# Optimization experiments

Measured on AMD Instinct MI355X. Metric: run time of the kernel, lower is better.

Reference implementation:

```python
import jax, jax.numpy as jnp
import numpy as np

SLOPE = 0.2  # leaky_relu_slope for both LVC block and kernel predictor (passed through)
DILATIONS = (1, 3, 9, 27)
HOP = 256
STRIDE = 8
IN_CH = 32
KSZ = 3  # conv_kernel_size


def conv1d(x, w, b, dilation=1, padding=0):
    # x: (B,C,T), w: (O,I,K) torch layout
    y = jax.lax.conv_general_dilated(
        x, w, window_strides=(1,), padding=[(padding, padding)],
        rhs_dilation=(dilation,), dimension_numbers=('NCH', 'OIH', 'NCH'))
    return y + b[None, :, None]


def conv_transpose1d(x, w, b, stride, padding, output_padding=0):
    # w: torch ConvTranspose1d layout (Cin, Cout, K)
    w_ = jnp.flip(w, -1).transpose(1, 0, 2)  # (Cout, Cin, K)
    K = w.shape[2]
    pad = (K - 1 - padding, K - 1 - padding + output_padding)
    y = jax.lax.conv_general_dilated(
        x, w_, window_strides=(1,), padding=[pad],
        lhs_dilation=(stride,), dimension_numbers=('NCH', 'OIH', 'NCH'))
    return y + b[None, :, None]


def lrelu(x, slope=SLOPE):
    return jnp.where(x >= 0, x, slope * x)


def location_variable_convolution(x, kernel, bias, hop):
    # x: (B,C,T), kernel: (B,C,O,k,L), bias: (B,O,L); T == L*hop; dilation==1 path
    B, C, T = x.shape
    _, _, O, k, L = kernel.shape
    pad = (k - 1) // 2
    xp = jnp.pad(x, ((0, 0), (0, 0), (pad, pad)))
    # gather per-segment sliding windows: (L, hop, k) index into time axis
    idx = (jnp.arange(L)[:, None, None] * hop
           + jnp.arange(hop)[None, :, None]
           + jnp.arange(k)[None, None, :])
    xw = xp[:, :, idx]  # (B, C, L, hop, k)
    o = jnp.einsum('bclsk,bcokl->bols', xw, kernel)  # (B, O, L, hop)
    o = o + bias[:, :, :, None]
    return o.reshape(B, O, L * hop)


def kernel_predictor(spec, kp_in_w, kp_in_b, rb_w1, rb_b1, rb_w2, rb_b2,
                     kern_w, kern_b, bias_w, bias_b):
    B, _, L = spec.shape
    h = conv1d(spec, kp_in_w, kp_in_b, padding=2)  # k=5, pad=2
    for i in range(3):  # num_blocks = 3
        r = h
        h = conv1d(h, rb_w1[i], rb_b1[i], padding=1)
        h = lrelu(h)
        h = conv1d(h, rb_w2[i], rb_b2[i], padding=1)
        h = lrelu(h) + r
    kh = conv1d(h, kern_w, kern_b, padding=1)
    bh = conv1d(h, bias_w, bias_b, padding=1)
    n_layers = len(DILATIONS)
    kernels = kh.reshape(B, n_layers, IN_CH, 2 * IN_CH, KSZ, L)
    biases = bh.reshape(B, n_layers, 2 * IN_CH, L)
    return kernels, biases


def reference(hidden_states, spectrogram, convt_w, convt_b, kp_in_w, kp_in_b,
              rb_w1, rb_b1, rb_w2, rb_b2, kern_w, kern_b, bias_w, bias_b,
              lvc_w, lvc_b):
    h = conv_transpose1d(hidden_states, convt_w, convt_b,
                         stride=STRIDE, padding=STRIDE // 2 + STRIDE % 2,
                         output_padding=STRIDE % 2)
    kernels, biases = kernel_predictor(spectrogram, kp_in_w, kp_in_b,
                                       rb_w1, rb_b1, rb_w2, rb_b2,
                                       kern_w, kern_b, bias_w, bias_b)
    for i, d in enumerate(DILATIONS):
        r = h
        h = lrelu(h)
        h = conv1d(h, lvc_w[i], lvc_b[i], dilation=d, padding=d * (KSZ - 1) // 2)
        h = lrelu(h)
        h = location_variable_convolution(h, kernels[:, i], biases[:, i], HOP)
        h = jax.nn.sigmoid(h[:, :IN_CH, :]) * jnp.tanh(h[:, IN_CH:, :]) + r
    return h


def setup_inputs() -> dict:
    key = jax.random.key(0)
    ks = jax.random.split(key, 12)
    B, COND, L, H = 4, 100, 256, 64
    T = L * HOP  # 65536 output samples
    s = jnp.float32(0.02)
    d = {}
    d['hidden_states'] = jax.random.normal(ks[0], (B, IN_CH, T // STRIDE), jnp.float32)
    d['spectrogram'] = jax.random.normal(ks[1], (B, COND, L), jnp.float32)
    d['convt_w'] = jax.random.normal(ks[2], (IN_CH, IN_CH, 2 * STRIDE), jnp.float32) * s
    d['convt_b'] = jnp.zeros((IN_CH,), jnp.float32)
    d['kp_in_w'] = jax.random.normal(ks[3], (H, COND, 5), jnp.float32) * s
    d['kp_in_b'] = jnp.zeros((H,), jnp.float32)
    d['rb_w1'] = jax.random.normal(ks[4], (3, H, H, 3), jnp.float32) * s
    d['rb_b1'] = jnp.zeros((3, H), jnp.float32)
    d['rb_w2'] = jax.random.normal(ks[5], (3, H, H, 3), jnp.float32) * s
    d['rb_b2'] = jnp.zeros((3, H), jnp.float32)
    KC = IN_CH * 2 * IN_CH * KSZ * len(DILATIONS)  # 24576
    d['kern_w'] = jax.random.normal(ks[6], (KC, H, 3), jnp.float32) * s
    d['kern_b'] = jnp.zeros((KC,), jnp.float32)
    BC = 2 * IN_CH * len(DILATIONS)  # 256
    d['bias_w'] = jax.random.normal(ks[7], (BC, H, 3), jnp.float32) * s
    d['bias_b'] = jnp.zeros((BC,), jnp.float32)
    d['lvc_w'] = jax.random.normal(ks[8], (len(DILATIONS), IN_CH, IN_CH, 3), jnp.float32) * s
    d['lvc_b'] = jnp.zeros((len(DILATIONS), IN_CH), jnp.float32)
    return d
```

## Files before the change

kernel.cpp:

```cpp
#include <hip/hip_runtime.h>
#include <math.h>

#define NB 4
#define T 65536
#define TIN 8192
#define LL 256
#define KCL 6144

__device__ __forceinline__ float lrelu_f(float v) { return v >= 0.f ? v : 0.2f * v; }

union Phase1LDS {
    struct { float xs[32][264]; float wm[64][128]; } cvt;
    struct { float hs[64][56]; float xsp[20][56]; float wt[192][68]; } trk;
};

__global__ void __launch_bounds__(512) phase1(
    const float* __restrict__ x, const float* __restrict__ cw,
    const float* __restrict__ cbias, float* __restrict__ hout,
    const float* __restrict__ spec,
    const float* __restrict__ kp_in_w, const float* __restrict__ kp_in_b,
    const float* __restrict__ rb_w1, const float* __restrict__ rb_b1,
    const float* __restrict__ rb_w2, const float* __restrict__ rb_b2,
    float* __restrict__ kp_h) {
    __shared__ Phase1LDS u;
    const int bid = blockIdx.x;
    const int tid = threadIdx.x;
    const int lane = tid & 63, wv = tid >> 6;

    if (bid < 264) {
        const int bx = bid % 33;
        const int rr = bid / 33;
        const int mtp = rr & 1;
        const int b = rr >> 1;
        const int s0base = bx * 256;
        float (*xs)[264] = u.cvt.xs;
        float (*wm)[128] = u.cvt.wm;

        const float* xb = x + (size_t)b * 32 * TIN;
        for (int idx = tid; idx < 32 * 64; idx += 512) {
            int c = idx >> 6, q = idx & 63;
            int p = s0base + q * 4;
            float4 v = (p + 3 < TIN) ? *(const float4*)(xb + c * TIN + p)
                                     : make_float4(0.f, 0.f, 0.f, 0.f);
            *(float4*)&xs[c][4 + 4 * q] = v;
        }
        if (tid < 32) {
            int p = s0base - 1;
            xs[tid][3] = (p >= 0) ? xb[tid * TIN + p] : 0.f;
        }
        for (int idx = tid; idx < 8192; idx += 512) {
            int i = idx >> 7, mm = idx & 127;
            int oo = mtp * 16 + (mm >> 3), k0 = mm & 7;
            wm[i][mm] = (i < 32) ? cw[i * 512 + oo * 16 + k0]
                                 : cw[(i - 32) * 512 + oo * 16 + k0 + 8];
        }
        __syncthreads();

        float acc[2][8][4];
#pragma unroll
        for (int ol = 0; ol < 2; ++ol) {
            float bo = cbias[mtp * 16 + wv * 2 + ol];
#pragma unroll
            for (int k0 = 0; k0 < 8; ++k0)
#pragma unroll
                for (int si = 0; si < 4; ++si) acc[ol][k0][si] = bo;
        }

        for (int c = 0; c < 32; ++c) {
            float xm1[4], x0[4];
#pragma unroll
            for (int si = 0; si < 4; ++si) {
                xm1[si] = xs[c][lane + si * 64 + 3];
                x0[si]  = xs[c][lane + si * 64 + 4];
            }
            float w0[16], w1[16];
#pragma unroll
            for (int q = 0; q < 4; ++q) {
                *(float4*)&w0[q * 4] = *(const float4*)&wm[c][wv * 16 + q * 4];
                *(float4*)&w1[q * 4] = *(const float4*)&wm[32 + c][wv * 16 + q * 4];
            }
#pragma unroll
            for (int ol = 0; ol < 2; ++ol)
#pragma unroll
                for (int k0 = 0; k0 < 8; ++k0)
#pragma unroll
                    for (int si = 0; si < 4; ++si)
                        acc[ol][k0][si] += x0[si] * w0[ol * 8 + k0] + xm1[si] * w1[ol * 8 + k0];
        }

#pragma unroll
        for (int ol = 0; ol < 2; ++ol) {
            float* ob = hout + ((size_t)b * 32 + mtp * 16 + wv * 2 + ol) * T;
#pragma unroll
            for (int si = 0; si < 4; ++si) {
                int tb = (s0base + lane + si * 64) * 8 - 4;
                if (tb >= 0 && tb < T)
                    *(float4*)(ob + tb) = make_float4(acc[ol][0][si], acc[ol][1][si],
                                                      acc[ol][2][si], acc[ol][3][si]);
                if (tb + 4 >= 0 && tb + 4 < T)
                    *(float4*)(ob + tb + 4) = make_float4(acc[ol][4][si], acc[ol][5][si],
                                                          acc[ol][6][si], acc[ol][7][si]);
            }
        }
        return;
    }

    const int tb = bid - 264;
    const int lq = tb & 7, b = tb >> 3;
    const int j = lane;
    const int oc0 = wv * 8;
    const int l0 = lq * 32;
    const int labs = l0 - 9 + j;
    const bool lvalid = (labs >= 0 && labs < 256);

    float (*hs)[56] = u.trk.hs;
    float (*xsp)[56] = u.trk.xsp;
    float (*wt)[68] = u.trk.wt;

    float pw[24];
    float px[3];

    auto pf_kpin = [&](int cc) {
#pragma unroll
        for (int t = 0; t < 13; ++t) {
            int idx = t * 512 + tid;
            pw[t] = 0.f;
            if (idx < 6400) pw[t] = kp_in_w[(size_t)(idx / 100) * 500 + cc * 100 + (idx % 100)];
        }
    };
    auto wr_kpin = [&]() {
#pragma unroll
        for (int t = 0; t < 13; ++t) {
            int idx = t * 512 + tid;
            if (idx < 6400) wt[idx % 100][idx / 100] = pw[t];
        }
    };
    auto pf_xsp = [&](int cc) {
#pragma unroll
        for (int t = 0; t < 3; ++t) {
            int idx = t * 512 + tid;
            px[t] = 0.f;
            if (idx < 1120) {
                int c = idx / 56, jj = idx - c * 56;
                int l = l0 - 9 + jj;
                if (l >= 0 && l < 256)
                    px[t] = spec[((size_t)b * 100 + cc * 20 + c) * LL + l];
            }
        }
    };
    auto wr_xsp = [&]() {
#pragma unroll
        for (int t = 0; t < 3; ++t) {
            int idx = t * 512 + tid;
            if (idx < 1120) xsp[idx / 56][idx % 56] = px[t];
        }
    };
    auto pf_w192 = [&](const float* src) {
#pragma unroll
        for (int t = 0; t < 24; ++t) pw[t] = src[t * 512 + tid];
    };
    auto wr_w192 = [&]() {
#pragma unroll
        for (int t = 0; t < 24; ++t) {
            int idx = t * 512 + tid;
            wt[idx % 192][idx / 192] = pw[t];
        }
    };
    auto conv64 = [&](int jlo, int jhi, const float* bptr, float* a) {
#pragma unroll
        for (int oi = 0; oi < 8; ++oi) a[oi] = bptr[oc0 + oi];
        if (j >= jlo && j < jhi) {
            for (int c = 0; c < 64; ++c) {
                float x0 = hs[c][j - 1], x1 = hs[c][j], x2 = hs[c][j + 1];
#pragma unroll
                for (int k = 0; k < 3; ++k) {
                    float xk = (k == 0) ? x0 : (k == 1) ? x1 : x2;
                    float w8[8];
                    *(float4*)&w8[0] = *(const float4*)&wt[c * 3 + k][oc0];
                    *(float4*)&w8[4] = *(const float4*)&wt[c * 3 + k][oc0 + 4];
#pragma unroll
                    for (int oi = 0; oi < 8; ++oi) a[oi] += xk * w8[oi];
                }
            }
        }
    };

    pf_kpin(0); pf_xsp(0);
    wr_kpin(); wr_xsp();
    __syncthreads();

    float acc[8];
#pragma unroll
    for (int oi = 0; oi < 8; ++oi) acc[oi] = kp_in_b[oc0 + oi];

    for (int cc = 0; cc < 5; ++cc) {
        if (cc < 4) { pf_kpin(cc + 1); pf_xsp(cc + 1); }
        else        { pf_w192(rb_w1); }
        if (j >= 2 && j < 48) {
            for (int c = 0; c < 20; ++c) {
                float x5[5];
#pragma unroll
                for (int u2 = 0; u2 < 5; ++u2) x5[u2] = xsp[c][j - 2 + u2];
#pragma unroll
                for (int k = 0; k < 5; ++k) {
                    float w8[8];
                    *(float4*)&w8[0] = *(const float4*)&wt[c * 5 + k][oc0];
                    *(float4*)&w8[4] = *(const float4*)&wt[c * 5 + k][oc0 + 4];
#pragma unroll
                    for (int oi = 0; oi < 8; ++oi) acc[oi] += x5[k] * w8[oi];
                }
            }
        }
        if (cc == 4 && j >= 2 && j < 48) {
#pragma unroll
            for (int oi = 0; oi < 8; ++oi) hs[oc0 + oi][j] = lvalid ? acc[oi] : 0.f;
        }
        __syncthreads();
        if (cc < 4) { wr_kpin(); wr_xsp(); }
        else        { wr_w192(); }
        __syncthreads();
    }

    for (int i = 0; i < 3; ++i) {
        const int jlo1 = 3 + 2 * i, jhi1 = 47 - 2 * i;
        const int jlo2 = jlo1 + 1, jhi2 = jhi1 - 1;
        float r[8];
        if (j >= jlo2 && j < jhi2) {
#pragma unroll
            for (int oi = 0; oi < 8; ++oi) r[oi] = hs[oc0 + oi][j];
        }
        pf_w192(rb_w2 + (size_t)i * 12288);
        float a1[8];
        conv64(jlo1, jhi1, rb_b1 + i * 64, a1);
        __syncthreads();
        if (j >= jlo1 && j < jhi1) {
#pragma unroll
            for (int oi = 0; oi < 8; ++oi) hs[oc0 + oi][j] = lvalid ? lrelu_f(a1[oi]) : 0.f;
        }
        wr_w192();
        __syncthreads();
        if (i < 2) pf_w192(rb_w1 + (size_t)(i + 1) * 12288);
        float a2[8];
        conv64(jlo2, jhi2, rb_b2 + i * 64, a2);
        __syncthreads();
        if (j >= jlo2 && j < jhi2) {
#pragma unroll
            for (int oi = 0; oi < 8; ++oi) hs[oc0 + oi][j] = lvalid ? (lrelu_f(a2[oi]) + r[oi]) : 0.f;
        }
        if (i < 2) wr_w192();
        __syncthreads();
    }

    for (int idx = tid; idx < 64 * 32; idx += 512) {
        int c = idx >> 5, jj = idx & 31;
        kp_h[((size_t)b * 64 + c) * LL + l0 + jj] = hs[c][9 + jj];
    }
}

__global__ void __launch_bounds__(256, 3) kern_head(const float* __restrict__ kp_h,
                                                    const float* __restrict__ kw,
                                                    const float* __restrict__ kb,
                                                    const float* __restrict__ bias_w,
                                                    const float* __restrict__ bias_b,
                                                    float* __restrict__ kh,
                                                    float* __restrict__ bh, int layer) {
    const int bx = blockIdx.x, b = blockIdx.y;
    const bool isbias = (bx >= 192);
    const int tid = threadIdx.x, lane = tid & 63, wv = tid >> 6;
    __shared__ float xs[32][264];
    __shared__ float ws[96][36];

    int g = 0, oc0 = 0, ci = 0, kk = 0, ocb0 = 0;
    const float* wsrc;
    size_t wrow0;
    int wstride;
    if (!isbias) {
        g = bx >> 1; oc0 = (bx & 1) * 32;
        ci = g / 3; kk = g - ci * 3;
        wsrc = kw + (size_t)layer * KCL * 192;
        wrow0 = (size_t)((ci * 64 + oc0) * 3 + kk) * 192;
        wstride = 576;
    } else {
        ocb0 = (bx - 192) * 32;
        wsrc = bias_w;
        wrow0 = (size_t)ocb0 * 192;
        wstride = 192;
    }

    float acc[8][4];
#pragma unroll
    for (int oi = 0; oi < 8; ++oi) {
        float bv = isbias ? bias_b[ocb0 + wv * 8 + oi]
                          : kb[layer * KCL + (ci * 64 + oc0 + wv * 8 + oi) * 3 + kk];
#pragma unroll
        for (int si = 0; si < 4; ++si) acc[oi][si] = bv;
    }

    for (int half = 0; half < 2; ++half) {
        const int hc0 = half * 32;
        __syncthreads();
        for (int idx = tid; idx < 32 * 64; idx += 256) {
            int c = idx >> 6, q = idx & 63;
            *(float4*)&xs[c][4 + 4 * q] =
                *(const float4*)(kp_h + ((size_t)b * 64 + hc0 + c) * LL + 4 * q);
        }
        if (tid < 32) { xs[tid][3] = 0.f; xs[tid][260] = 0.f; }
        for (int idx = tid; idx < 3072; idx += 256) {
            int ocl = idx / 96, jj = idx - ocl * 96;
            ws[jj][ocl] = wsrc[wrow0 + (size_t)ocl * wstride + hc0 * 3 + jj];
        }
        __syncthreads();
        for (int c = 0; c < 32; ++c) {
#pragma unroll
            for (int t = 0; t < 3; ++t) {
                float wv8[8];
                *(float4*)&wv8[0] = *(const float4*)&ws[c * 3 + t][wv * 8];
                *(float4*)&wv8[4] = *(const float4*)&ws[c * 3 + t][wv * 8 + 4];
                float xv[4];
#pragma unroll
                for (int si = 0; si < 4; ++si) xv[si] = xs[c][lane + si * 64 + t + 3];
#pragma unroll
                for (int oi = 0; oi < 8; ++oi)
#pragma unroll
                    for (int si = 0; si < 4; ++si)
                        acc[oi][si] += wv8[oi] * xv[si];
            }
        }
    }

    if (!isbias) {
#pragma unroll
        for (int si = 0; si < 4; ++si) {
            int l = lane + si * 64;
            float* op = kh + ((size_t)b * LL + l) * KCL + g * 64 + oc0 + wv * 8;
            *(float4*)(op)     = make_float4(acc[0][si], acc[1][si], acc[2][si], acc[3][si]);
            *(float4*)(op + 4) = make_float4(acc[4][si], acc[5][si], acc[6][si], acc[7][si]);
        }
    } else {
#pragma unroll
        for (int oi = 0; oi < 8; ++oi) {
            float* op = bh + ((size_t)b * 256 + ocb0 + wv * 8 + oi) * LL;
#pragma unroll
            for (int si = 0; si < 4; ++si)
                op[lane + si * 64] = acc[oi][si];
        }
    }
}

__global__ void __launch_bounds__(512, 4) layer_fused(
    const float* __restrict__ kh, const float* __restrict__ bh,
    const float* __restrict__ w, const float* __restrict__ bias,
    const float* __restrict__ hin, float* __restrict__ hout,
    int layer, int dil) {
    const int l = blockIdx.x, b = blockIdx.y;
    const int tid = threadIdx.x, lane = tid & 63, wv = tid >> 6;
    const int t0 = l * 256;
    __shared__ float xh[32][316];
    __shared__ float ks[KCL];
    __shared__ float ws[96][36];

    const float* hb = hin + (size_t)b * 32 * T;
    for (int idx = tid; idx < 32 * 64; idx += 512) {
        int c = idx >> 6, q = idx & 63;
        float4 v = *(const float4*)(hb + (size_t)c * T + t0 + 4 * q);
        *(float4*)&xh[c][32 + 4 * q] = make_float4(lrelu_f(v.x), lrelu_f(v.y),
                                                   lrelu_f(v.z), lrelu_f(v.w));
    }
    for (int idx = tid; idx < 32 * 60; idx += 512) {
        int c = idx / 60, r = idx - c * 60;
        int jj = (r < 32) ? r : (256 + r);
        int t = t0 + jj - 32;
        xh[c][jj] = (t >= 0 && t < T) ? lrelu_f(hb[(size_t)c * T + t]) : 0.f;
    }
    {
        const float4* kp = (const float4*)(kh + ((size_t)b * LL + l) * KCL);
        float4* kd = (float4*)ks;
        for (int idx = tid; idx < KCL / 4; idx += 512) kd[idx] = kp[idx];
    }
    for (int idx = tid; idx < 3072; idx += 512) {
        int oc = idx / 96, ck = idx - oc * 96;
        ws[ck][oc] = w[oc * 96 + ck];
    }
    __syncthreads();

    const int oc4 = wv * 4;
    float yv[5][4];
    {
        float a[5][4];
#pragma unroll
        for (int oi = 0; oi < 4; ++oi) {
            float bv = bias[oc4 + oi];
#pragma unroll
            for (int si = 0; si < 5; ++si) a[si][oi] = bv;
        }
        for (int c = 0; c < 32; ++c) {
#pragma unroll
            for (int k = 0; k < 3; ++k) {
                float4 wq = *(const float4*)&ws[c * 3 + k][oc4];
                float xv[5];
#pragma unroll
                for (int si = 0; si < 5; ++si) {
                    int col = lane + si * 64;
                    int colc = (col < 258) ? col : 257;
                    xv[si] = xh[c][colc + 31 + (k - 1) * dil];
                }
#pragma unroll
                for (int si = 0; si < 5; ++si) {
                    a[si][0] += xv[si] * wq.x;
                    a[si][1] += xv[si] * wq.y;
                    a[si][2] += xv[si] * wq.z;
                    a[si][3] += xv[si] * wq.w;
                }
            }
        }
#pragma unroll
        for (int si = 0; si < 5; ++si) {
            int t = t0 - 1 + lane + si * 64;
            bool tval = (t >= 0 && t < T);
#pragma unroll
            for (int oi = 0; oi < 4; ++oi)
                yv[si][oi] = tval ? lrelu_f(a[si][oi]) : 0.f;
        }
    }
    __syncthreads();

#pragma unroll
    for (int si = 0; si < 5; ++si) {
        int col = lane + si * 64;
        if (col < 258) {
#pragma unroll
            for (int oi = 0; oi < 4; ++oi) xh[oc4 + oi][col + 31] = yv[si][oi];
        }
    }
    __syncthreads();

    const int oc8 = (wv & 3) * 8;
    const int sh  = wv >> 2;
    float acc_a[8][2], acc_g[8][2];
#pragma unroll
    for (int oi = 0; oi < 8; ++oi) {
        float ba = bh[((size_t)b * 256 + layer * 64 + oc8 + oi) * LL + l];
        float bg = bh[((size_t)b * 256 + layer * 64 + 32 + oc8 + oi) * LL + l];
#pragma unroll
        for (int si = 0; si < 2; ++si) { acc_a[oi][si] = ba; acc_g[oi][si] = bg; }
    }

    for (int c = 0; c < 32; ++c) {
#pragma unroll
        for (int k = 0; k < 3; ++k) {
            const float* kr = ks + (c * 3 + k) * 64;
            float wa[8], wg[8];
            *(float4*)&wa[0] = *(const float4*)(kr + oc8);
            *(float4*)&wa[4] = *(const float4*)(kr + oc8 + 4);
            *(float4*)&wg[0] = *(const float4*)(kr + 32 + oc8);
            *(float4*)&wg[4] = *(const float4*)(kr + 32 + oc8 + 4);
            float xv2[2];
#pragma unroll
            for (int si = 0; si < 2; ++si) {
                int s = lane + (sh * 2 + si) * 64;
                xv2[si] = xh[c][s + k + 31];
            }
#pragma unroll
            for (int oi = 0; oi < 8; ++oi)
#pragma unroll
                for (int si = 0; si < 2; ++si) {
                    acc_a[oi][si] += wa[oi] * xv2[si];
                    acc_g[oi][si] += wg[oi] * xv2[si];
                }
        }
    }

#pragma unroll
    for (int oi = 0; oi < 8; ++oi) {
        const float* hip = hin + ((size_t)b * 32 + oc8 + oi) * T + t0;
        float* hop = hout + ((size_t)b * 32 + oc8 + oi) * T + t0;
#pragma unroll
        for (int si = 0; si < 2; ++si) {
            int s = lane + (sh * 2 + si) * 64;
            float a = acc_a[oi][si], g = acc_g[oi][si];
            float sg = 1.f / (1.f + __expf(-a));
            float th = tanhf(g);
            hop[s] = sg * th + hip[s];
        }
    }
}

extern "C" void kernel_launch(void* const* d_in, const int* in_sizes, int n_in,
                              void* d_out, int out_size, void* d_ws, size_t ws_size,
                              hipStream_t stream) {
    const float* hidden  = (const float*)d_in[0];
    const float* spec    = (const float*)d_in[1];
    const float* convt_w = (const float*)d_in[2];
    const float* convt_b = (const float*)d_in[3];
    const float* kp_in_w = (const float*)d_in[4];
    const float* kp_in_b = (const float*)d_in[5];
    const float* rb_w1   = (const float*)d_in[6];
    const float* rb_b1   = (const float*)d_in[7];
    const float* rb_w2   = (const float*)d_in[8];
    const float* rb_b2   = (const float*)d_in[9];
    const float* kern_w  = (const float*)d_in[10];
    const float* kern_b  = (const float*)d_in[11];
    const float* bias_w  = (const float*)d_in[12];
    const float* bias_b  = (const float*)d_in[13];
    const float* lvc_w   = (const float*)d_in[14];
    const float* lvc_b   = (const float*)d_in[15];

    float* wsp = (float*)d_ws;
    float* h_ws     = wsp;
    float* kh_layer = h_ws + (size_t)NB * 32 * T;
    float* bh       = kh_layer + (size_t)NB * LL * KCL;
    float* kp_h     = bh + (size_t)NB * 256 * LL;

    float* h0 = (float*)d_out;
    float* h1 = h_ws;

    phase1<<<dim3(296), 512, 0, stream>>>(hidden, convt_w, convt_b, h0,
                                          spec, kp_in_w, kp_in_b,
                                          rb_w1, rb_b1, rb_w2, rb_b2, kp_h);

    static const int dil[4] = {1, 3, 9, 27};
    float* hin = h0;
    float* hout = h1;
    for (int layer = 0; layer < 4; ++layer) {
        kern_head<<<dim3(layer == 0 ? 200 : 192, NB), 256, 0, stream>>>(
            kp_h, kern_w, kern_b, bias_w, bias_b, kh_layer, bh, layer);
        layer_fused<<<dim3(LL, NB), 512, 0, stream>>>(
            kh_layer, bh, lvc_w + (size_t)layer * 32 * 32 * 3, lvc_b + layer * 32,
            hin, hout, layer, dil[layer]);
        float* tmp = hin; hin = hout; hout = tmp;
    }
}
```

Measured before the change: 721.6 us.

## Split kernel-predictor trunk into per-wave small tiles with pre-transposed global weights

```diff
diff --git a/kernel.cpp b/kernel.cpp
--- a/kernel.cpp
+++ b/kernel.cpp
@@ -9,252 +9,234 @@
 
 __device__ __forceinline__ float lrelu_f(float v) { return v >= 0.f ? v : 0.2f * v; }
 
+__global__ void __launch_bounds__(256) prep1(
+    const float* __restrict__ rb_w1, const float* __restrict__ rb_w2,
+    const float* __restrict__ kp_in_w,
+    float* __restrict__ trb, float* __restrict__ tkpin) {
+  __shared__ float t[64][193];
+  const int bid = blockIdx.x, tid = threadIdx.x;
+  if (bid < 6) {
+    int i = bid >> 1, which = bid & 1;
+    const float* src = (which ? rb_w2 : rb_w1) + (size_t)i * 12288;
+    float* dst = trb + (size_t)bid * 12288;
+    for (int idx = tid; idx < 64 * 192; idx += 256) {
+      int o = idx / 192, J = idx % 192;
+      t[o][J] = src[(size_t)o * 192 + J];
+    }
+    __syncthreads();
+    for (int idx = tid; idx < 64 * 192; idx += 256) {
+      int J = idx >> 6, o = idx & 63;
+      dst[(size_t)J * 64 + o] = t[o][J];
+    }
+  } else {
+    for (int idx = tid; idx < 500 * 64; idx += 256) {
+      int row = idx >> 6, o = idx & 63;
+      tkpin[idx] = kp_in_w[o * 500 + row];
+    }
+  }
+}
+
 union Phase1LDS {
-    struct { float xs[32][264]; float wm[64][128]; } cvt;
-    struct { float hs[64][56]; float xsp[20][56]; float wt[192][68]; } trk;
+  struct { float xs[32][264]; float wm[64][128]; } cvt;
+  struct { float hs[4][64][20]; float xsp[4][100][24]; } trk;
 };
 
 __global__ void __launch_bounds__(512) phase1(
     const float* __restrict__ x, const float* __restrict__ cw,
     const float* __restrict__ cbias, float* __restrict__ hout,
     const float* __restrict__ spec,
-    const float* __restrict__ kp_in_w, const float* __restrict__ kp_in_b,
-    const float* __restrict__ rb_w1, const float* __restrict__ rb_b1,
-    const float* __restrict__ rb_w2, const float* __restrict__ rb_b2,
-    float* __restrict__ kp_h) {
-    __shared__ Phase1LDS u;
-    const int bid = blockIdx.x;
-    const int tid = threadIdx.x;
-    const int lane = tid & 63, wv = tid >> 6;
-
-    if (bid < 264) {
-        const int bx = bid % 33;
-        const int rr = bid / 33;
-        const int mtp = rr & 1;
-        const int b = rr >> 1;
-        const int s0base = bx * 256;
-        float (*xs)[264] = u.cvt.xs;
-        float (*wm)[128] = u.cvt.wm;
-
-        const float* xb = x + (size_t)b * 32 * TIN;
-        for (int idx = tid; idx < 32 * 64; idx += 512) {
-            int c = idx >> 6, q = idx & 63;
-            int p = s0base + q * 4;
-            float4 v = (p + 3 < TIN) ? *(const float4*)(xb + c * TIN + p)
-                                     : make_float4(0.f, 0.f, 0.f, 0.f);
-            *(float4*)&xs[c][4 + 4 * q] = v;
-        }
-        if (tid < 32) {
-            int p = s0base - 1;
-            xs[tid][3] = (p >= 0) ? xb[tid * TIN + p] : 0.f;
-        }
-        for (int idx = tid; idx < 8192; idx += 512) {
-            int i = idx >> 7, mm = idx & 127;
-            int oo = mtp * 16 + (mm >> 3), k0 = mm & 7;
-            wm[i][mm] = (i < 32) ? cw[i * 512 + oo * 16 + k0]
-                                 : cw[(i - 32) * 512 + oo * 16 + k0 + 8];
-        }
-        __syncthreads();
-
-        float acc[2][8][4];
-#pragma unroll
-        for (int ol = 0; ol < 2; ++ol) {
-            float bo = cbias[mtp * 16 + wv * 2 + ol];
-#pragma unroll
-            for (int k0 = 0; k0 < 8; ++k0)
-#pragma unroll
-                for (int si = 0; si < 4; ++si) acc[ol][k0][si] = bo;
-        }
-
-        for (int c = 0; c < 32; ++c) {
-            float xm1[4], x0[4];
-#pragma unroll
-            for (int si = 0; si < 4; ++si) {
-                xm1[si] = xs[c][lane + si * 64 + 3];
-                x0[si]  = xs[c][lane + si * 64 + 4];
-            }
-            float w0[16], w1[16];
-#pragma unroll
-            for (int q = 0; q < 4; ++q) {
-                *(float4*)&w0[q * 4] = *(const float4*)&wm[c][wv * 16 + q * 4];
-                *(float4*)&w1[q * 4] = *(const float4*)&wm[32 + c][wv * 16 + q * 4];
-            }
-#pragma unroll
-            for (int ol = 0; ol < 2; ++ol)
-#pragma unroll
-                for (int k0 = 0; k0 < 8; ++k0)
-#pragma unroll
-                    for (int si = 0; si < 4; ++si)
-                        acc[ol][k0][si] += x0[si] * w0[ol * 8 + k0] + xm1[si] * w1[ol * 8 + k0];
-        }
-
-#pragma unroll
-        for (int ol = 0; ol < 2; ++ol) {
-            float* ob = hout + ((size_t)b * 32 + mtp * 16 + wv * 2 + ol) * T;
-#pragma unroll
-            for (int si = 0; si < 4; ++si) {
-                int tb = (s0base + lane + si * 64) * 8 - 4;
-                if (tb >= 0 && tb < T)
-                    *(float4*)(ob + tb) = make_float4(acc[ol][0][si], acc[ol][1][si],
-                                                      acc[ol][2][si], acc[ol][3][si]);
-                if (tb + 4 >= 0 && tb + 4 < T)
-                    *(float4*)(ob + tb + 4) = make_float4(acc[ol][4][si], acc[ol][5][si],
-                                                          acc[ol][6][si], acc[ol][7][si]);
-            }
-        }
-        return;
-    }
-
-    const int tb = bid - 264;
-    const int lq = tb & 7, b = tb >> 3;
-    const int j = lane;
-    const int oc0 = wv * 8;
-    const int l0 = lq * 32;
-    const int labs = l0 - 9 + j;
-    const bool lvalid = (labs >= 0 && labs < 256);
-
-    float (*hs)[56] = u.trk.hs;
-    float (*xsp)[56] = u.trk.xsp;
-    float (*wt)[68] = u.trk.wt;
-
-    float pw[24];
-    float px[3];
-
-    auto pf_kpin = [&](int cc) {
-#pragma unroll
-        for (int t = 0; t < 13; ++t) {
-            int idx = t * 512 + tid;
-            pw[t] = 0.f;
-            if (idx < 6400) pw[t] = kp_in_w[(size_t)(idx / 100) * 500 + cc * 100 + (idx % 100)];
-        }
-    };
-    auto wr_kpin = [&]() {
-#pragma unroll
-        for (int t = 0; t < 13; ++t) {
-            int idx = t * 512 + tid;
-            if (idx < 6400) wt[idx % 100][idx / 100] = pw[t];
-        }
-    };
-    auto pf_xsp = [&](int cc) {
-#pragma unroll
-        for (int t = 0; t < 3; ++t) {
-            int idx = t * 512 + tid;
-            px[t] = 0.f;
-            if (idx < 1120) {
-                int c = idx / 56, jj = idx - c * 56;
-                int l = l0 - 9 + jj;
-                if (l >= 0 && l < 256)
-                    px[t] = spec[((size_t)b * 100 + cc * 20 + c) * LL + l];
-            }
-        }
-    };
-    auto wr_xsp = [&]() {
-#pragma unroll
-        for (int t = 0; t < 3; ++t) {
-            int idx = t * 512 + tid;
-            if (idx < 1120) xsp[idx / 56][idx % 56] = px[t];
-        }
-    };
-    auto pf_w192 = [&](const float* src) {
-#pragma unroll
-        for (int t = 0; t < 24; ++t) pw[t] = src[t * 512 + tid];
-    };
-    auto wr_w192 = [&]() {
-#pragma unroll
-        for (int t = 0; t < 24; ++t) {
-            int idx = t * 512 + tid;
-            wt[idx % 192][idx / 192] = pw[t];
-        }
-    };
-    auto conv64 = [&](int jlo, int jhi, const float* bptr, float* a) {
-#pragma unroll
-        for (int oi = 0; oi < 8; ++oi) a[oi] = bptr[oc0 + oi];
-        if (j >= jlo && j < jhi) {
-            for (int c = 0; c < 64; ++c) {
-                float x0 = hs[c][j - 1], x1 = hs[c][j], x2 = hs[c][j + 1];
-#pragma unroll
-                for (int k = 0; k < 3; ++k) {
-                    float xk = (k == 0) ? x0 : (k == 1) ? x1 : x2;
-                    float w8[8];
-                    *(float4*)&w8[0] = *(const float4*)&wt[c * 3 + k][oc0];
-                    *(float4*)&w8[4] = *(const float4*)&wt[c * 3 + k][oc0 + 4];
-#pragma unroll
-                    for (int oi = 0; oi < 8; ++oi) a[oi] += xk * w8[oi];
-                }
-            }
-        }
-    };
-
-    pf_kpin(0); pf_xsp(0);
-    wr_kpin(); wr_xsp();
-    __syncthreads();
-
-    float acc[8];
-#pragma unroll
-    for (int oi = 0; oi < 8; ++oi) acc[oi] = kp_in_b[oc0 + oi];
-
-    for (int cc = 0; cc < 5; ++cc) {
-        if (cc < 4) { pf_kpin(cc + 1); pf_xsp(cc + 1); }
-        else        { pf_w192(rb_w1); }
-        if (j >= 2 && j < 48) {
-            for (int c = 0; c < 20; ++c) {
-                float x5[5];
-#pragma unroll
-                for (int u2 = 0; u2 < 5; ++u2) x5[u2] = xsp[c][j - 2 + u2];
-#pragma unroll
-                for (int k = 0; k < 5; ++k) {
-                    float w8[8];
-                    *(float4*)&w8[0] = *(const float4*)&wt[c * 5 + k][oc0];
-                    *(float4*)&w8[4] = *(const float4*)&wt[c * 5 + k][oc0 + 4];
-#pragma unroll
-                    for (int oi = 0; oi < 8; ++oi) acc[oi] += x5[k] * w8[oi];
-                }
-            }
-        }
-        if (cc == 4 && j >= 2 && j < 48) {
-#pragma unroll
-            for (int oi = 0; oi < 8; ++oi) hs[oc0 + oi][j] = lvalid ? acc[oi] : 0.f;
-        }
-        __syncthreads();
-        if (cc < 4) { wr_kpin(); wr_xsp(); }
-        else        { wr_w192(); }
-        __syncthreads();
-    }
-
-    for (int i = 0; i < 3; ++i) {
-        const int jlo1 = 3 + 2 * i, jhi1 = 47 - 2 * i;
-        const int jlo2 = jlo1 + 1, jhi2 = jhi1 - 1;
-        float r[8];
-        if (j >= jlo2 && j < jhi2) {
-#pragma unroll
-            for (int oi = 0; oi < 8; ++oi) r[oi] = hs[oc0 + oi][j];
-        }
-        pf_w192(rb_w2 + (size_t)i * 12288);
-        float a1[8];
-        conv64(jlo1, jhi1, rb_b1 + i * 64, a1);
-        __syncthreads();
-        if (j >= jlo1 && j < jhi1) {
-#pragma unroll
-            for (int oi = 0; oi < 8; ++oi) hs[oc0 + oi][j] = lvalid ? lrelu_f(a1[oi]) : 0.f;
-        }
-        wr_w192();
-        __syncthreads();
-        if (i < 2) pf_w192(rb_w1 + (size_t)(i + 1) * 12288);
-        float a2[8];
-        conv64(jlo2, jhi2, rb_b2 + i * 64, a2);
-        __syncthreads();
-        if (j >= jlo2 && j < jhi2) {
-#pragma unroll
-            for (int oi = 0; oi < 8; ++oi) hs[oc0 + oi][j] = lvalid ? (lrelu_f(a2[oi]) + r[oi]) : 0.f;
-        }
-        if (i < 2) wr_w192();
-        __syncthreads();
-    }
-
-    for (int idx = tid; idx < 64 * 32; idx += 512) {
-        int c = idx >> 5, jj = idx & 31;
-        kp_h[((size_t)b * 64 + c) * LL + l0 + jj] = hs[c][9 + jj];
-    }
+    const float* __restrict__ tkpin, const float* __restrict__ kp_in_b,
+    const float* __restrict__ trb, const float* __restrict__ rb_b1,
+    const float* __restrict__ rb_b2, float* __restrict__ kp_h) {
+  __shared__ Phase1LDS sm;
+  const int bid = blockIdx.x;
+  const int tid = threadIdx.x;
+  const int lane = tid & 63, wv = tid >> 6;
+
+  if (bid < 64) {
+    if (wv >= 4) return;
+    const int unit = bid * 4 + wv;
+    const int b = unit >> 6;
+    const int chunk = unit & 63;
+    const int l0 = chunk * 4;
+    const int og = lane >> 1;
+    const int colg = lane & 1;
+    const int colg8 = colg * 8;
+    const int obase = og * 2;
+    float (*hsu)[20] = sm.trk.hs[wv];
+    float (*xspu)[24] = sm.trk.xsp[wv];
+
+    for (int i = lane; i < 64 * 20; i += 64) ((float*)hsu)[i] = 0.f;
+
+    for (int i = lane; i < 100 * 24; i += 64) {
+      int cin = i / 24, cx = i - cin * 24;
+      float v = 0.f;
+      if (cx < 20) {
+        int labs = l0 - 8 + cx;
+        if (labs >= 0 && labs < 256)
+          v = spec[((size_t)b * 100 + cin) * LL + labs];
+      }
+      xspu[cin][cx] = v;
+    }
+
+    float hcur[2][8];
+    {
+      float acc[2][8];
+      float2 bb = *(const float2*)(kp_in_b + obase);
+#pragma unroll
+      for (int q = 0; q < 8; ++q) { acc[0][q] = bb.x; acc[1][q] = bb.y; }
+#pragma unroll 2
+      for (int cin = 0; cin < 100; ++cin) {
+        float x12[12];
+        *(float4*)&x12[0] = *(const float4*)&xspu[cin][colg8];
+        *(float4*)&x12[4] = *(const float4*)&xspu[cin][colg8 + 4];
+        *(float4*)&x12[8] = *(const float4*)&xspu[cin][colg8 + 8];
+        const float* wp = tkpin + (size_t)(cin * 5) * 64 + obase;
+#pragma unroll
+        for (int k = 0; k < 5; ++k) {
+          float2 w = *(const float2*)(wp + k * 64);
+#pragma unroll
+          for (int q = 0; q < 8; ++q) {
+            acc[0][q] += x12[q + k] * w.x;
+            acc[1][q] += x12[q + k] * w.y;
+          }
+        }
+      }
+#pragma unroll
+      for (int oi = 0; oi < 2; ++oi)
+#pragma unroll
+        for (int q = 0; q < 8; ++q) {
+          int rel = colg8 + q, labs = l0 - 6 + rel;
+          float v = (labs >= 0 && labs < 256) ? acc[oi][q] : 0.f;
+          hcur[oi][q] = v;
+          hsu[obase + oi][rel + 1] = v;
+        }
+    }
+
+    for (int cv = 0; cv < 6; ++cv) {
+      const float* wb = trb + (size_t)cv * 12288;
+      const float* bp = (cv & 1) ? rb_b2 + (cv >> 1) * 64 : rb_b1 + (cv >> 1) * 64;
+      float2 bb = *(const float2*)(bp + obase);
+      float acc[2][8];
+#pragma unroll
+      for (int q = 0; q < 8; ++q) { acc[0][q] = bb.x; acc[1][q] = bb.y; }
+#pragma unroll 2
+      for (int c = 0; c < 64; ++c) {
+        float x10[10];
+        *(float4*)&x10[0] = *(const float4*)&hsu[c][colg8];
+        *(float4*)&x10[4] = *(const float4*)&hsu[c][colg8 + 4];
+        *(float2*)&x10[8] = *(const float2*)&hsu[c][colg8 + 8];
+        const float* wp = wb + (size_t)(c * 192) + obase;
+        float2 w0 = *(const float2*)(wp);
+        float2 w1 = *(const float2*)(wp + 64);
+        float2 w2 = *(const float2*)(wp + 128);
+#pragma unroll
+        for (int q = 0; q < 8; ++q) {
+          acc[0][q] += x10[q] * w0.x + x10[q + 1] * w1.x + x10[q + 2] * w2.x;
+          acc[1][q] += x10[q] * w0.y + x10[q + 1] * w1.y + x10[q + 2] * w2.y;
+        }
+      }
+      const int lo = cv + 1, hi = 15 - cv;
+#pragma unroll
+      for (int oi = 0; oi < 2; ++oi)
+#pragma unroll
+        for (int q = 0; q < 8; ++q) {
+          int rel = colg8 + q, labs = l0 - 6 + rel;
+          float v = lrelu_f(acc[oi][q]);
+          if (cv & 1) v += hcur[oi][q];
+          bool ok = (rel >= lo) && (rel < hi) && (labs >= 0) && (labs < 256);
+          v = ok ? v : 0.f;
+          if (cv & 1) hcur[oi][q] = v;
+          if (cv < 5) hsu[obase + oi][rel + 1] = v;
+        }
+    }
+
+#pragma unroll
+    for (int oi = 0; oi < 2; ++oi)
+#pragma unroll
+      for (int q = 0; q < 8; ++q) {
+        int rel = colg8 + q;
+        if (rel >= 6 && rel < 10)
+          kp_h[((size_t)b * 64 + obase + oi) * LL + l0 + rel - 6] = hcur[oi][q];
+      }
+    return;
+  }
+
+  const int cb = bid - 64;
+  const int bx = cb % 33;
+  const int rr = cb / 33;
+  const int mtp = rr & 1;
+  const int b = rr >> 1;
+  const int s0base = bx * 256;
+  float (*xs)[264] = sm.cvt.xs;
+  float (*wm)[128] = sm.cvt.wm;
+
+  const float* xb = x + (size_t)b * 32 * TIN;
+  for (int idx = tid; idx < 32 * 64; idx += 512) {
+    int c = idx >> 6, q = idx & 63;
+    int p = s0base + q * 4;
+    float4 v = (p + 3 < TIN) ? *(const float4*)(xb + c * TIN + p)
+                             : make_float4(0.f, 0.f, 0.f, 0.f);
+    *(float4*)&xs[c][4 + 4 * q] = v;
+  }
+  if (tid < 32) {
+    int p = s0base - 1;
+    xs[tid][3] = (p >= 0) ? xb[tid * TIN + p] : 0.f;
+  }
+  for (int idx = tid; idx < 8192; idx += 512) {
+    int i = idx >> 7, mm = idx & 127;
+    int oo = mtp * 16 + (mm >> 3), k0 = mm & 7;
+    wm[i][mm] = (i < 32) ? cw[i * 512 + oo * 16 + k0]
+                         : cw[(i - 32) * 512 + oo * 16 + k0 + 8];
+  }
+  __syncthreads();
+
+  float acc[2][8][4];
+#pragma unroll
+  for (int ol = 0; ol < 2; ++ol) {
+    float bo = cbias[mtp * 16 + wv * 2 + ol];
+#pragma unroll
+    for (int k0 = 0; k0 < 8; ++k0)
+#pragma unroll
+      for (int si = 0; si < 4; ++si) acc[ol][k0][si] = bo;
+  }
+
+  for (int c = 0; c < 32; ++c) {
+    float xm1[4], x0[4];
+#pragma unroll
+    for (int si = 0; si < 4; ++si) {
+      xm1[si] = xs[c][lane + si * 64 + 3];
+      x0[si]  = xs[c][lane + si * 64 + 4];
+    }
+    float w0[16], w1[16];
+#pragma unroll
+    for (int q = 0; q < 4; ++q) {
+      *(float4*)&w0[q * 4] = *(const float4*)&wm[c][wv * 16 + q * 4];
+      *(float4*)&w1[q * 4] = *(const float4*)&wm[32 + c][wv * 16 + q * 4];
+    }
+#pragma unroll
+    for (int ol = 0; ol < 2; ++ol)
+#pragma unroll
+      for (int k0 = 0; k0 < 8; ++k0)
+#pragma unroll
+        for (int si = 0; si < 4; ++si)
+          acc[ol][k0][si] += x0[si] * w0[ol * 8 + k0] + xm1[si] * w1[ol * 8 + k0];
+  }
+
+#pragma unroll
+  for (int ol = 0; ol < 2; ++ol) {
+    float* ob = hout + ((size_t)b * 32 + mtp * 16 + wv * 2 + ol) * T;
+#pragma unroll
+    for (int si = 0; si < 4; ++si) {
+      int tb = (s0base + lane + si * 64) * 8 - 4;
+      if (tb >= 0 && tb < T)
+        *(float4*)(ob + tb) = make_float4(acc[ol][0][si], acc[ol][1][si],
+                                          acc[ol][2][si], acc[ol][3][si]);
+      if (tb + 4 >= 0 && tb + 4 < T)
+        *(float4*)(ob + tb + 4) = make_float4(acc[ol][4][si], acc[ol][5][si],
+                                              acc[ol][6][si], acc[ol][7][si]);
+    }
+  }
 }
 
 __global__ void __launch_bounds__(256, 3) kern_head(const float* __restrict__ kp_h,
@@ -510,13 +492,17 @@
     float* kh_layer = h_ws + (size_t)NB * 32 * T;
     float* bh       = kh_layer + (size_t)NB * LL * KCL;
     float* kp_h     = bh + (size_t)NB * 256 * LL;
+    float* trb      = kp_h + (size_t)NB * 64 * LL;
+    float* tkpin    = trb + (size_t)6 * 192 * 64;
 
     float* h0 = (float*)d_out;
     float* h1 = h_ws;
 
-    phase1<<<dim3(296), 512, 0, stream>>>(hidden, convt_w, convt_b, h0,
-                                          spec, kp_in_w, kp_in_b,
-                                          rb_w1, rb_b1, rb_w2, rb_b2, kp_h);
+    prep1<<<dim3(7), 256, 0, stream>>>(rb_w1, rb_w2, kp_in_w, trb, tkpin);
+
+    phase1<<<dim3(328), 512, 0, stream>>>(hidden, convt_w, convt_b, h0,
+                                          spec, tkpin, kp_in_b,
+                                          trb, rb_b1, rb_b2, kp_h);
 
     static const int dil[4] = {1, 3, 9, 27};
     float* hin = h0;
```

After: 781.4 us. 1.08x slower.

## Overlap next-layer kernel prediction with current LVC layer in one launch

Applied to the files above, without the earlier changes.

```diff
diff --git a/kernel.cpp b/kernel.cpp
--- a/kernel.cpp
+++ b/kernel.cpp
@@ -257,19 +257,15 @@
     }
 }
 
-__global__ void __launch_bounds__(256, 3) kern_head(const float* __restrict__ kp_h,
-                                                    const float* __restrict__ kw,
-                                                    const float* __restrict__ kb,
-                                                    const float* __restrict__ bias_w,
-                                                    const float* __restrict__ bias_b,
-                                                    float* __restrict__ kh,
-                                                    float* __restrict__ bh, int layer) {
-    const int bx = blockIdx.x, b = blockIdx.y;
+__device__ __forceinline__ void khead_core(
+    int bx, int b, int tid,
+    const float* __restrict__ kp_h, const float* __restrict__ kw,
+    const float* __restrict__ kb, const float* __restrict__ bias_w,
+    const float* __restrict__ bias_b, float* __restrict__ kh,
+    float* __restrict__ bh, int layer,
+    float (*xs)[264], float (*ws)[36]) {
     const bool isbias = (bx >= 192);
-    const int tid = threadIdx.x, lane = tid & 63, wv = tid >> 6;
-    __shared__ float xs[32][264];
-    __shared__ float ws[96][36];
-
+    const int lane = tid & 63, wv = tid >> 6;
     int g = 0, oc0 = 0, ci = 0, kk = 0, ocb0 = 0;
     const float* wsrc;
     size_t wrow0;
@@ -286,12 +282,13 @@
         wrow0 = (size_t)ocb0 * 192;
         wstride = 192;
     }
-
-    float acc[8][4];
-#pragma unroll
-    for (int oi = 0; oi < 8; ++oi) {
-        float bv = isbias ? bias_b[ocb0 + wv * 8 + oi]
-                          : kb[layer * KCL + (ci * 64 + oc0 + wv * 8 + oi) * 3 + kk];
+    const int oc4w = wv * 4;
+
+    float acc[4][4];
+#pragma unroll
+    for (int oi = 0; oi < 4; ++oi) {
+        float bv = isbias ? bias_b[ocb0 + oc4w + oi]
+                          : kb[layer * KCL + (ci * 64 + oc0 + oc4w + oi) * 3 + kk];
 #pragma unroll
         for (int si = 0; si < 4; ++si) acc[oi][si] = bv;
     }
@@ -299,13 +296,13 @@
     for (int half = 0; half < 2; ++half) {
         const int hc0 = half * 32;
         __syncthreads();
-        for (int idx = tid; idx < 32 * 64; idx += 256) {
+        for (int idx = tid; idx < 32 * 64; idx += 512) {
             int c = idx >> 6, q = idx & 63;
             *(float4*)&xs[c][4 + 4 * q] =
                 *(const float4*)(kp_h + ((size_t)b * 64 + hc0 + c) * LL + 4 * q);
         }
         if (tid < 32) { xs[tid][3] = 0.f; xs[tid][260] = 0.f; }
-        for (int idx = tid; idx < 3072; idx += 256) {
+        for (int idx = tid; idx < 3072; idx += 512) {
             int ocl = idx / 96, jj = idx - ocl * 96;
             ws[jj][ocl] = wsrc[wrow0 + (size_t)ocl * wstride + hc0 * 3 + jj];
         }
@@ -313,17 +310,17 @@
         for (int c = 0; c < 32; ++c) {
 #pragma unroll
             for (int t = 0; t < 3; ++t) {
-                float wv8[8];
-                *(float4*)&wv8[0] = *(const float4*)&ws[c * 3 + t][wv * 8];
-                *(float4*)&wv8[4] = *(const float4*)&ws[c * 3 + t][wv * 8 + 4];
+                float4 w4 = *(const float4*)&ws[c * 3 + t][oc4w];
                 float xv[4];
 #pragma unroll
                 for (int si = 0; si < 4; ++si) xv[si] = xs[c][lane + si * 64 + t + 3];
 #pragma unroll
-                for (int oi = 0; oi < 8; ++oi)
-#pragma unroll
-                    for (int si = 0; si < 4; ++si)
-                        acc[oi][si] += wv8[oi] * xv[si];
+                for (int si = 0; si < 4; ++si) {
+                    acc[0][si] += w4.x * xv[si];
+                    acc[1][si] += w4.y * xv[si];
+                    acc[2][si] += w4.z * xv[si];
+                    acc[3][si] += w4.w * xv[si];
+                }
             }
         }
     }
@@ -332,14 +329,13 @@
 #pragma unroll
         for (int si = 0; si < 4; ++si) {
             int l = lane + si * 64;
-            float* op = kh + ((size_t)b * LL + l) * KCL + g * 64 + oc0 + wv * 8;
-            *(float4*)(op)     = make_float4(acc[0][si], acc[1][si], acc[2][si], acc[3][si]);
-            *(float4*)(op + 4) = make_float4(acc[4][si], acc[5][si], acc[6][si], acc[7][si]);
+            float* op = kh + ((size_t)b * LL + l) * KCL + g * 64 + oc0 + oc4w;
+            *(float4*)op = make_float4(acc[0][si], acc[1][si], acc[2][si], acc[3][si]);
         }
     } else {
 #pragma unroll
-        for (int oi = 0; oi < 8; ++oi) {
-            float* op = bh + ((size_t)b * 256 + ocb0 + wv * 8 + oi) * LL;
+        for (int oi = 0; oi < 4; ++oi) {
+            float* op = bh + ((size_t)b * 256 + ocb0 + oc4w + oi) * LL;
 #pragma unroll
             for (int si = 0; si < 4; ++si)
                 op[lane + si * 64] = acc[oi][si];
@@ -347,17 +343,26 @@
     }
 }
 
-__global__ void __launch_bounds__(512, 4) layer_fused(
+__global__ void __launch_bounds__(512, 2) kern_head512(
+    const float* __restrict__ kp_h, const float* __restrict__ kw,
+    const float* __restrict__ kb, const float* __restrict__ bias_w,
+    const float* __restrict__ bias_b, float* __restrict__ kh,
+    float* __restrict__ bh, int layer) {
+    __shared__ float xs[32][264];
+    __shared__ float ws[96][36];
+    khead_core(blockIdx.x, blockIdx.y, threadIdx.x, kp_h, kw, kb, bias_w, bias_b,
+               kh, bh, layer, xs, ws);
+}
+
+__device__ __forceinline__ void lf_core(
+    int l, int b, int tid,
     const float* __restrict__ kh, const float* __restrict__ bh,
     const float* __restrict__ w, const float* __restrict__ bias,
     const float* __restrict__ hin, float* __restrict__ hout,
-    int layer, int dil) {
-    const int l = blockIdx.x, b = blockIdx.y;
-    const int tid = threadIdx.x, lane = tid & 63, wv = tid >> 6;
+    int layer, int dil,
+    float (*xh)[316], float* ks, float (*ws)[36]) {
+    const int lane = tid & 63, wv = tid >> 6;
     const int t0 = l * 256;
-    __shared__ float xh[32][316];
-    __shared__ float ks[KCL];
-    __shared__ float ws[96][36];
 
     const float* hb = hin + (size_t)b * 32 * T;
     for (int idx = tid; idx < 32 * 64; idx += 512) {
@@ -482,6 +487,41 @@
             float th = tanhf(g);
             hop[s] = sg * th + hip[s];
         }
+    }
+}
+
+union FusedLDS {
+    struct { float xh[32][316]; float ks[KCL]; float ws[96][36]; } lf;
+    struct { float xs[32][264]; float ws[96][36]; } kh;
+};
+
+__global__ void __launch_bounds__(512, 2) fused(
+    const float* __restrict__ kp_h, const float* __restrict__ kw,
+    const float* __restrict__ kb, const float* __restrict__ bias_w,
+    const float* __restrict__ bias_b,
+    const float* __restrict__ kh_rd, float* __restrict__ kh_wr,
+    float* __restrict__ bh,
+    const float* __restrict__ lvcw, const float* __restrict__ lvcb,
+    const float* __restrict__ hin, float* __restrict__ hout,
+    int lf_layer, int dil, int kh_on) {
+    __shared__ FusedLDS u;
+    const int g = blockIdx.x;
+    const int tid = threadIdx.x;
+    if (kh_on) {
+        const int r = g % 7, q7 = g / 7;
+        if (r < 3) {
+            const int ukh = q7 * 3 + r;
+            const int bx = ukh % 192, b = ukh / 192;
+            khead_core(bx, b, tid, kp_h, kw, kb, bias_w, bias_b,
+                       kh_wr, bh, lf_layer + 1, u.kh.xs, u.kh.ws);
+            return;
+        }
+        const int ulf = q7 * 4 + (r - 3);
+        lf_core(ulf & 255, ulf >> 8, tid, kh_rd, bh, lvcw, lvcb,
+                hin, hout, lf_layer, dil, u.lf.xh, u.lf.ks, u.lf.ws);
+    } else {
+        lf_core(g & 255, g >> 8, tid, kh_rd, bh, lvcw, lvcb,
+                hin, hout, lf_layer, dil, u.lf.xh, u.lf.ks, u.lf.ws);
     }
 }
 
@@ -505,11 +545,19 @@
     const float* lvc_w   = (const float*)d_in[14];
     const float* lvc_b   = (const float*)d_in[15];
 
-    float* wsp = (float*)d_ws;
-    float* h_ws     = wsp;
-    float* kh_layer = h_ws + (size_t)NB * 32 * T;
-    float* bh       = kh_layer + (size_t)NB * LL * KCL;
-    float* kp_h     = bh + (size_t)NB * 256 * LL;
+    const size_t NH  = (size_t)NB * 32 * T;
+    const size_t NKH = (size_t)NB * LL * KCL;
+    const size_t NBH = (size_t)NB * 256 * LL;
+    const size_t NKP = (size_t)NB * 64 * LL;
+    const size_t need_pp = (NH + 2 * NKH + NBH + NKP) * sizeof(float);
+    const bool pp = ws_size >= need_pp;
+
+    float* wsp  = (float*)d_ws;
+    float* h_ws = wsp;
+    float* kh0  = h_ws + NH;
+    float* kh1  = pp ? (kh0 + NKH) : kh0;
+    float* bh   = (pp ? kh1 : kh0) + NKH;
+    float* kp_h = bh + NBH;
 
     float* h0 = (float*)d_out;
     float* h1 = h_ws;
@@ -518,15 +566,29 @@
                                           spec, kp_in_w, kp_in_b,
                                           rb_w1, rb_b1, rb_w2, rb_b2, kp_h);
 
+    kern_head512<<<dim3(200, NB), 512, 0, stream>>>(
+        kp_h, kern_w, kern_b, bias_w, bias_b, kh0, bh, 0);
+
     static const int dil[4] = {1, 3, 9, 27};
     float* hin = h0;
     float* hout = h1;
-    for (int layer = 0; layer < 4; ++layer) {
-        kern_head<<<dim3(layer == 0 ? 200 : 192, NB), 256, 0, stream>>>(
-            kp_h, kern_w, kern_b, bias_w, bias_b, kh_layer, bh, layer);
-        layer_fused<<<dim3(LL, NB), 512, 0, stream>>>(
-            kh_layer, bh, lvc_w + (size_t)layer * 32 * 32 * 3, lvc_b + layer * 32,
-            hin, hout, layer, dil[layer]);
+    for (int l = 0; l < 4; ++l) {
+        const float* rd = (l & 1) ? kh1 : kh0;
+        float* wr = (l & 1) ? kh0 : kh1;
+        if (pp && l < 3) {
+            fused<<<dim3(1792), 512, 0, stream>>>(
+                kp_h, kern_w, kern_b, bias_w, bias_b, rd, wr, bh,
+                lvc_w + (size_t)l * 32 * 32 * 3, lvc_b + l * 32,
+                hin, hout, l, dil[l], 1);
+        } else {
+            fused<<<dim3(1024), 512, 0, stream>>>(
+                kp_h, kern_w, kern_b, bias_w, bias_b, rd, (float*)rd, bh,
+                lvc_w + (size_t)l * 32 * 32 * 3, lvc_b + l * 32,
+                hin, hout, l, dil[l], 0);
+            if (!pp && l < 3)
+                kern_head512<<<dim3(192, NB), 512, 0, stream>>>(
+                    kp_h, kern_w, kern_b, bias_w, bias_b, kh0, bh, l + 1);
+        }
         float* tmp = hin; hin = hout; hout = tmp;
     }
 }
```

Result: no change. 736.0 us (+2.0%).
